# Performance work log

Hardware: AMD Instinct MI355X
Metric: run time of the kernel (lower is better)

## Reference

```python
import jax, jax.numpy as jnp
import numpy as np

N_SLOTS, KEY_DIM, VAL_DIM = 8192, 64, 64
B, S, TOPK = 8, 2048, 8


def setup_inputs() -> dict:
    key = jax.random.key(0)
    k1, k2, k3, k4, k5 = jax.random.split(key, 5)
    queries = jax.random.normal(k1, (B, S, KEY_DIM), dtype=jnp.float32)
    keys_mem = jax.random.normal(k2, (N_SLOTS, KEY_DIM), dtype=jnp.float32) * 0.02
    vals_mem = jax.random.normal(k3, (N_SLOTS, VAL_DIM), dtype=jnp.float32) * 0.02
    fast_vals = jax.random.normal(k4, (N_SLOTS, VAL_DIM), dtype=jnp.float32) * 0.01
    timestamps = jax.random.uniform(k5, (N_SLOTS,), dtype=jnp.float32)
    return {
        "queries": queries,
        "keys_mem": keys_mem,
        "vals_mem": vals_mem,
        "fast_vals": fast_vals,
        "timestamps": timestamps,
        "topk": TOPK,
    }


def reference(queries, keys_mem, vals_mem, fast_vals, timestamps, topk):
    # sim: [B, S, n_slots], scaled dot-product vs. memory keys
    scale = keys_mem.shape[1] ** (-0.5)
    sim = jnp.einsum("bsd,nd->bsn", queries, keys_mem) * scale
    # topk indices computed on detached scores (torch uses sim.detach())
    _, idx = jax.lax.top_k(jax.lax.stop_gradient(sim), topk)  # idx: [B, S, k]
    # gather topk similarities (torch does this via one-hot * sim; same math)
    sim_topk = jnp.take_along_axis(sim, idx, axis=-1)  # [B, S, k]
    # effective memory = slow + fast store; gather rows (torch: one_hot @ memory)
    effective_memory = vals_mem + fast_vals  # [n_slots, val_dim]
    gathered_vals = effective_memory[idx]  # [B, S, k, val_dim]
    attn_weights = jax.nn.softmax(sim_topk, axis=-1)  # [B, S, k]
    weighted_vals = gathered_vals * attn_weights[..., None]  # [B, S, k, val_dim]
    ts_retrieved = timestamps[idx]  # [B, S, k]
    return weighted_vals, idx, ts_retrieved
```

## Files before the change

### kernel.cpp

```cpp
#include <hip/hip_runtime.h>
#include <math.h>

#define NQ      16384
#define NSLOTS  8192
#define D       64
#define K       8

#define WV_ELEMS  (NQ * K * D)
#define IDX_OFF   (WV_ELEMS)
#define TSO_OFF   (IDX_OFF + NQ * K)

#define QPB_P   32
#define BLOCK_P 512
#define HALVES  2
#define SPW_P   (NSLOTS / HALVES / 8)
#define ITERS_P (SPW_P / 32)

#define QPB_R   16
#define BLOCK_R 256

#define POOL_SHORT_OFF 1572864
#define WS_NEED_NEW  (4u * 1024u * 1024u)
#define WS_NEED_OLD  (3u * 1024u * 1024u)

using short8   = __attribute__((ext_vector_type(8))) short;
using ushort8  = __attribute__((ext_vector_type(8))) unsigned short;
using bf16x8   = __attribute__((ext_vector_type(8))) __bf16;
using f32x4    = __attribute__((ext_vector_type(4))) float;

#define MFMA_BF16(A, B, C) __builtin_amdgcn_mfma_f32_16x16x32_bf16((A), (B), (C), 0, 0, 0)

__device__ __forceinline__ bf16x8 load_frag(const unsigned short* p) {
    short8 s = *reinterpret_cast<const short8*>(p);
    return __builtin_bit_cast(bf16x8, s);
}

__device__ __forceinline__ float packkey(float s, int code) {
    unsigned u = __float_as_uint(s) & 0xFFFFE000u;
    return __uint_as_float(u | (unsigned)code);
}

__device__ __forceinline__ void ins8(float (&tv)[8], float key) {
    float k2 = fmaxf(key, tv[0]);
    float o0 = fminf(tv[1], k2);
    float o1 = __builtin_amdgcn_fmed3f(tv[1], tv[2], k2);
    float o2 = __builtin_amdgcn_fmed3f(tv[2], tv[3], k2);
    float o3 = __builtin_amdgcn_fmed3f(tv[3], tv[4], k2);
    float o4 = __builtin_amdgcn_fmed3f(tv[4], tv[5], k2);
    float o5 = __builtin_amdgcn_fmed3f(tv[5], tv[6], k2);
    float o6 = __builtin_amdgcn_fmed3f(tv[6], tv[7], k2);
    float o7 = fmaxf(tv[7], k2);
    tv[0]=o0; tv[1]=o1; tv[2]=o2; tv[3]=o3; tv[4]=o4; tv[5]=o5; tv[6]=o6; tv[7]=o7;
}

__device__ __forceinline__ void cs(float& a, float& b) {
    const float lo = fminf(a, b), hi = fmaxf(a, b);
    a = lo; b = hi;
}
__device__ __forceinline__ void sort_bitonic8(float (&v)[8]) {
    cs(v[0],v[4]); cs(v[1],v[5]); cs(v[2],v[6]); cs(v[3],v[7]);
    cs(v[0],v[2]); cs(v[1],v[3]); cs(v[4],v[6]); cs(v[5],v[7]);
    cs(v[0],v[1]); cs(v[2],v[3]); cs(v[4],v[5]); cs(v[6],v[7]);
}

__device__ __forceinline__ void csu(unsigned long long& a, unsigned long long& b) {
    const bool lt = a < b;
    const unsigned long long lo = lt ? a : b;
    const unsigned long long hi = lt ? b : a;
    a = lo; b = hi;
}
__device__ __forceinline__ void sort_bitonic8_u64(unsigned long long (&v)[8]) {
    csu(v[0],v[4]); csu(v[1],v[5]); csu(v[2],v[6]); csu(v[3],v[7]);
    csu(v[0],v[2]); csu(v[1],v[3]); csu(v[4],v[6]); csu(v[5],v[7]);
    csu(v[0],v[1]); csu(v[2],v[3]); csu(v[4],v[5]); csu(v[6],v[7]);
}

__device__ __forceinline__ unsigned short f2bf(float f) {
    unsigned u = __float_as_uint(f);
    return (unsigned short)((u + 0x7FFFu + ((u >> 16) & 1u)) >> 16);
}

__global__ __launch_bounds__(256)
void conv_kernel(const float* __restrict__ q, const float* __restrict__ k,
                 unsigned short* __restrict__ ws) {
    const int t = blockIdx.x * blockDim.x + threadIdx.x;
    if (t < 262144) {
        float4 v = reinterpret_cast<const float4*>(q)[t];
        unsigned long long r =
              (unsigned long long)f2bf(v.x * 0.125f)
            | ((unsigned long long)f2bf(v.y * 0.125f) << 16)
            | ((unsigned long long)f2bf(v.z * 0.125f) << 32)
            | ((unsigned long long)f2bf(v.w * 0.125f) << 48);
        reinterpret_cast<unsigned long long*>(ws + 524288)[t] = r;
    } else if (t < 393216) {
        const int i = t - 262144;
        float4 v = reinterpret_cast<const float4*>(k)[i];
        unsigned long long r =
              (unsigned long long)f2bf(v.x)
            | ((unsigned long long)f2bf(v.y) << 16)
            | ((unsigned long long)f2bf(v.z) << 32)
            | ((unsigned long long)f2bf(v.w) << 48);
        reinterpret_cast<unsigned long long*>(ws)[i] = r;
    }
}

__global__ __launch_bounds__(BLOCK_P, 8)
void ltm_prefilter_kernel(const unsigned short* __restrict__ kb,
                          const unsigned short* __restrict__ qb,
                          unsigned short* __restrict__ poolu)
{
    __shared__ float candk[QPB_P][68];

    const int tid  = threadIdx.x;
    const int lane = tid & 63;
    const int w    = tid >> 6;
    const int row  = lane & 15;
    const int g    = lane >> 4;
    const int g4   = g * 4;
    const int koff = g * 8;
    const int bid  = blockIdx.x;
    const int qbase = (bid >> 1) * QPB_P;
    const int half  = bid & 1;

    const unsigned short* qpA = qb + (size_t)(qbase + row) * D + koff;
    const bf16x8 bA0 = load_frag(qpA);
    const bf16x8 bA1 = load_frag(qpA + 32);
    const bf16x8 bB0 = load_frag(qpA + 16 * D);
    const bf16x8 bB1 = load_frag(qpA + 16 * D + 32);

    float tvA[8], tvB[8];
    #pragma unroll
    for (int i = 0; i < 8; ++i) { tvA[i] = -INFINITY; tvB[i] = -INFINITY; }

    const int wbase = half * (NSLOTS / HALVES) + w * SPW_P;
    int codeA = 8191 - (wbase + g4);

    for (int it = 0; it < ITERS_P; ++it) {
        const int s0 = wbase + it * 32;
        const unsigned short* p = kb + (size_t)(s0 + row) * D + koff;
        const bf16x8 a00 = load_frag(p);
        const bf16x8 a01 = load_frag(p + 32);
        const bf16x8 a10 = load_frag(p + 16 * D);
        const bf16x8 a11 = load_frag(p + 16 * D + 32);

        const f32x4 z = {0.f, 0.f, 0.f, 0.f};
        f32x4 c00 = MFMA_BF16(a00, bA0, z);  c00 = MFMA_BF16(a01, bA1, c00);
        f32x4 c01 = MFMA_BF16(a00, bB0, z);  c01 = MFMA_BF16(a01, bB1, c01);
        f32x4 c10 = MFMA_BF16(a10, bA0, z);  c10 = MFMA_BF16(a11, bA1, c10);
        f32x4 c11 = MFMA_BF16(a10, bB0, z);  c11 = MFMA_BF16(a11, bB1, c11);

        ins8(tvA, packkey(c00[0], codeA     ));
        ins8(tvA, packkey(c00[1], codeA -  1));
        ins8(tvA, packkey(c00[2], codeA -  2));
        ins8(tvA, packkey(c00[3], codeA -  3));
        ins8(tvA, packkey(c10[0], codeA - 16));
        ins8(tvA, packkey(c10[1], codeA - 17));
        ins8(tvA, packkey(c10[2], codeA - 18));
        ins8(tvA, packkey(c10[3], codeA - 19));
        ins8(tvB, packkey(c01[0], codeA     ));
        ins8(tvB, packkey(c01[1], codeA -  1));
        ins8(tvB, packkey(c01[2], codeA -  2));
        ins8(tvB, packkey(c01[3], codeA -  3));
        ins8(tvB, packkey(c11[0], codeA - 16));
        ins8(tvB, packkey(c11[1], codeA - 17));
        ins8(tvB, packkey(c11[2], codeA - 18));
        ins8(tvB, packkey(c11[3], codeA - 19));

        codeA -= 32;
    }

    {
        float sA[8], sB[8];
        #pragma unroll
        for (int j = 0; j < 8; ++j) {
            sA[j] = __shfl_xor(tvA[j], 32, 64);
            sB[j] = __shfl_xor(tvB[j], 32, 64);
        }
        float mA[8], mB[8];
        #pragma unroll
        for (int j = 0; j < 8; ++j) {
            mA[j] = fmaxf(tvA[j], sA[7 - j]);
            mB[j] = fmaxf(tvB[j], sB[7 - j]);
        }
        sort_bitonic8(mA);
        sort_bitonic8(mB);
        #pragma unroll
        for (int j = 0; j < 8; ++j) {
            sA[j] = __shfl_xor(mA[j], 16, 64);
            sB[j] = __shfl_xor(mB[j], 16, 64);
        }
        float fA[8], fB[8];
        #pragma unroll
        for (int j = 0; j < 8; ++j) {
            fA[j] = fmaxf(mA[j], sA[7 - j]);
            fB[j] = fmaxf(mB[j], sB[7 - j]);
        }
        sort_bitonic8(fA);
        sort_bitonic8(fB);
        if (g == 0) {
            #pragma unroll
            for (int j = 0; j < 8; ++j) {
                candk[row     ][w * 8 + j] = fA[j];
                candk[row + 16][w * 8 + j] = fB[j];
            }
        }
    }
    __syncthreads();

    if (tid < 256) {
        const int  ql = tid >> 3;
        const int  jj = tid & 7;
        const bool hi = (jj & 1) != 0;

        float v[8];
        #pragma unroll
        for (int i = 0; i < 8; ++i) v[i] = candk[ql][jj * 8 + i];

        {
            float sk[8], mk[8];
            #pragma unroll
            for (int i = 0; i < 8; ++i) sk[i] = __shfl_xor(v[i], 1, 64);
            #pragma unroll
            for (int i = 0; i < 8; ++i)
                mk[i] = hi ? fmaxf(v[i], sk[7 - i]) : fminf(v[i], sk[7 - i]);
            sort_bitonic8(mk);
            #pragma unroll
            for (int i = 0; i < 8; ++i) v[i] = mk[i];
        }
        #pragma unroll
        for (int rnd = 0; rnd < 2; ++rnd) {
            const int st = rnd ? 5 : 3;
            float sk[8], mk[8], sk2[8];
            #pragma unroll
            for (int i = 0; i < 8; ++i) sk[i] = __shfl_xor(v[i], st, 64);
            #pragma unroll
            for (int i = 0; i < 8; ++i) mk[i] = fmaxf(v[i], sk[7 - i]);
            #pragma unroll
            for (int i = 0; i < 8; ++i) sk2[i] = __shfl_xor(mk[i], 1, 64);
            #pragma unroll
            for (int i = 0; i < 8; ++i)
                mk[i] = hi ? fmaxf(mk[i], sk2[i]) : fminf(mk[i], sk2[i]);
            sort_bitonic8(mk);
            #pragma unroll
            for (int i = 0; i < 8; ++i) v[i] = mk[i];
        }
        if (jj < 2) {
            ushort8 o;
            #pragma unroll
            for (int i = 0; i < 8; ++i)
                o[i] = (unsigned short)(8191u - (__float_as_uint(v[i]) & 8191u));
            *reinterpret_cast<ushort8*>(
                poolu + ((size_t)(qbase + ql) * 32 + half * 16 + jj * 8)) = o;
        }
    }
}

__global__ __launch_bounds__(BLOCK_R, 4)
void ltm_rescore_kernel(const float* __restrict__ queries,
                        const float* __restrict__ keys_mem,
                        const float* __restrict__ vals_mem,
                        const float* __restrict__ fast_vals,
                        const float* __restrict__ timestamps,
                        const unsigned short* __restrict__ poolu,
                        float* __restrict__ out)
{
    const int tid = threadIdx.x;
    const int ql  = tid >> 4;
    const int l16 = tid & 15;
    const int sg  = l16 >> 2;
    const int ls4 = l16 & 3;
    const int q   = blockIdx.x * QPB_R + ql;

    float4 qv4[4];
    {
        const float4* qp = reinterpret_cast<const float4*>(queries) + (size_t)q * 16 + ls4 * 4;
        #pragma unroll
        for (int i = 0; i < 4; ++i) qv4[i] = qp[i];
    }

    unsigned long long tk[8];
    #pragma unroll
    for (int i = 0; i < 8; ++i) tk[i] = 0ull;

    #pragma unroll 4
    for (int jt = 0; jt < 8; ++jt) {
        const int sid = poolu[(size_t)q * 32 + sg * 8 + jt];
        const float4* kp = reinterpret_cast<const float4*>(keys_mem) + (size_t)sid * 16 + ls4 * 4;
        float p = 0.f;
        #pragma unroll
        for (int i = 0; i < 4; ++i) {
            const float4 kc = kp[i];
            p = fmaf(qv4[i].x, kc.x, p);
            p = fmaf(qv4[i].y, kc.y, p);
            p = fmaf(qv4[i].z, kc.z, p);
            p = fmaf(qv4[i].w, kc.w, p);
        }
        p += __shfl_xor(p, 1, 64);
        p += __shfl_xor(p, 2, 64);
        const float s = p * 0.125f;
        const unsigned u  = __float_as_uint(s);
        const unsigned ou = (u & 0x80000000u) ? ~u : (u | 0x80000000u);
        const unsigned long long key =
            ((unsigned long long)ou << 13) | (unsigned)(8191 - sid);
        if (key > tk[0]) {
            tk[0] = key;
            #pragma unroll
            for (int uu = 0; uu < 7; ++uu) {
                const bool sw = tk[uu] > tk[uu + 1];
                const unsigned long long x = sw ? tk[uu + 1] : tk[uu];
                const unsigned long long y = sw ? tk[uu]     : tk[uu + 1];
                tk[uu] = x; tk[uu + 1] = y;
            }
        }
    }

    #pragma unroll
    for (int st = 4; st <= 8; st <<= 1) {
        unsigned long long sk[8], mk[8];
        #pragma unroll
        for (int j = 0; j < 8; ++j) sk[j] = __shfl_xor(tk[j], st, 64);
        #pragma unroll
        for (int j = 0; j < 8; ++j) {
            const unsigned long long a = tk[j], b = sk[7 - j];
            mk[j] = a > b ? a : b;
        }
        sort_bitonic8_u64(mk);
        #pragma unroll
        for (int j = 0; j < 8; ++j) tk[j] = mk[j];
    }

    float wv[K]; int wi[K];
    #pragma unroll
    for (int r = 0; r < K; ++r) {
        const unsigned long long best = tk[7 - r];
        const int      sid = 8191 - (int)(best & 8191ull);
        const unsigned ou  = (unsigned)(best >> 13);
        const unsigned ub  = (ou & 0x80000000u) ? (ou & 0x7FFFFFFFu) : ~ou;
        wv[r] = __uint_as_float(ub);
        wi[r] = sid;
    }
    const float m = wv[0];
    float e[K]; float sum = 0.f;
    #pragma unroll
    for (int r = 0; r < K; ++r) { e[r] = expf(wv[r] - m); sum += e[r]; }
    const float inv = 1.f / sum;

    {
        const int   r   = l16 >> 1;
        const int   h   = l16 & 1;
        const int   id  = wi[r];
        const float wgt = e[r] * inv;
        const float4* vp = reinterpret_cast<const float4*>(vals_mem)  + (size_t)id * 16 + h * 8;
        const float4* fp = reinterpret_cast<const float4*>(fast_vals) + (size_t)id * 16 + h * 8;
        float4* op = reinterpret_cast<float4*>(out) + ((size_t)(q * K + r)) * 16 + h * 8;
        #pragma unroll
        for (int i = 0; i < 8; ++i) {
            const float4 a = vp[i];
            const float4 b = fp[i];
            float4 c;
            c.x = (a.x + b.x) * wgt;
            c.y = (a.y + b.y) * wgt;
            c.z = (a.z + b.z) * wgt;
            c.w = (a.w + b.w) * wgt;
            op[i] = c;
        }
        if (l16 < 8) {
            out[IDX_OFF + (size_t)q * K + l16] = (float)wi[l16];
        } else {
            const int r2 = l16 - 8;
            out[TSO_OFF + (size_t)q * K + r2] = timestamps[wi[r2]];
        }
    }
}

#define QPB    32
#define BLOCK  512
#define WAVES  8
#define SPW    (NSLOTS / WAVES)
#define ITERS  (SPW / 32)

__global__ __launch_bounds__(BLOCK, 4)
void ltm_mfma_kernel(const float* __restrict__ queries,
                     const float* __restrict__ keys_mem,
                     const float* __restrict__ vals_mem,
                     const float* __restrict__ fast_vals,
                     const float* __restrict__ timestamps,
                     const unsigned short* __restrict__ kb,
                     const unsigned short* __restrict__ qb,
                     float* __restrict__ out)
{
    __shared__ float candk[QPB][68];

    const int tid  = threadIdx.x;
    const int lane = tid & 63;
    const int w    = tid >> 6;
    const int row  = lane & 15;
    const int g    = lane >> 4;
    const int g4   = g * 4;
    const int koff = g * 8;
    const int qbase = blockIdx.x * QPB;

    const unsigned short* qpA = qb + (size_t)(qbase + row) * D + koff;
    const bf16x8 bA0 = load_frag(qpA);
    const bf16x8 bA1 = load_frag(qpA + 32);
    const bf16x8 bB0 = load_frag(qpA + 16 * D);
    const bf16x8 bB1 = load_frag(qpA + 16 * D + 32);

    float tvA[8], tvB[8];
    #pragma unroll
    for (int i = 0; i < 8; ++i) { tvA[i] = -INFINITY; tvB[i] = -INFINITY; }

    const int wbase = w * SPW;
    const unsigned short* kp0 = kb + (size_t)(wbase + row) * D + koff;
    bf16x8 a00 = load_frag(kp0);
    bf16x8 a01 = load_frag(kp0 + 32);
    bf16x8 a10 = load_frag(kp0 + 16 * D);
    bf16x8 a11 = load_frag(kp0 + 16 * D + 32);

    int codeA = 8191 - (wbase + g4);

    #pragma unroll 2
    for (int it = 0; it < ITERS; ++it) {
        const int snext = wbase + (it + 1) * 32;
        const unsigned short* np_ = kb + (size_t)(snext + row) * D + koff;
        bf16x8 n00 = load_frag(np_);
        bf16x8 n01 = load_frag(np_ + 32);
        bf16x8 n10 = load_frag(np_ + 16 * D);
        bf16x8 n11 = load_frag(np_ + 16 * D + 32);

        const f32x4 z = {0.f, 0.f, 0.f, 0.f};
        f32x4 c00 = MFMA_BF16(a00, bA0, z);  c00 = MFMA_BF16(a01, bA1, c00);
        f32x4 c01 = MFMA_BF16(a00, bB0, z);  c01 = MFMA_BF16(a01, bB1, c01);
        f32x4 c10 = MFMA_BF16(a10, bA0, z);  c10 = MFMA_BF16(a11, bA1, c10);
        f32x4 c11 = MFMA_BF16(a10, bB0, z);  c11 = MFMA_BF16(a11, bB1, c11);

        ins8(tvA, packkey(c00[0], codeA     ));
        ins8(tvA, packkey(c00[1], codeA -  1));
        ins8(tvA, packkey(c00[2], codeA -  2));
        ins8(tvA, packkey(c00[3], codeA -  3));
        ins8(tvA, packkey(c10[0], codeA - 16));
        ins8(tvA, packkey(c10[1], codeA - 17));
        ins8(tvA, packkey(c10[2], codeA - 18));
        ins8(tvA, packkey(c10[3], codeA - 19));
        ins8(tvB, packkey(c01[0], codeA     ));
        ins8(tvB, packkey(c01[1], codeA -  1));
        ins8(tvB, packkey(c01[2], codeA -  2));
        ins8(tvB, packkey(c01[3], codeA -  3));
        ins8(tvB, packkey(c11[0], codeA - 16));
        ins8(tvB, packkey(c11[1], codeA - 17));
        ins8(tvB, packkey(c11[2], codeA - 18));
        ins8(tvB, packkey(c11[3], codeA - 19));

        codeA -= 32;
        a00 = n00; a01 = n01; a10 = n10; a11 = n11;
    }

    {
        float sA[8], sB[8];
        #pragma unroll
        for (int j = 0; j < 8; ++j) {
            sA[j] = __shfl_xor(tvA[j], 32, 64);
            sB[j] = __shfl_xor(tvB[j], 32, 64);
        }
        float mA[8], mB[8];
        #pragma unroll
        for (int j = 0; j < 8; ++j) {
            mA[j] = fmaxf(tvA[j], sA[7 - j]);
            mB[j] = fmaxf(tvB[j], sB[7 - j]);
        }
        sort_bitonic8(mA);
        sort_bitonic8(mB);
        #pragma unroll
        for (int j = 0; j < 8; ++j) {
            sA[j] = __shfl_xor(mA[j], 16, 64);
            sB[j] = __shfl_xor(mB[j], 16, 64);
        }
        if (g == 0) {
            #pragma unroll
            for (int j = 0; j < 8; ++j) {
                candk[row     ][w * 8 + j] = fmaxf(mA[j], sA[7 - j]);
                candk[row + 16][w * 8 + j] = fmaxf(mB[j], sB[7 - j]);
            }
        }
    }
    __syncthreads();

    const int ql  = tid >> 4;
    const int l16 = tid & 15;
    const int sg  = l16 >> 2;
    const int ls4 = l16 & 3;
    const int q   = qbase + ql;

    float4 qv4[4];
    {
        const float4* qp = reinterpret_cast<const float4*>(queries) + (size_t)q * 16 + ls4 * 4;
        #pragma unroll
        for (int i = 0; i < 4; ++i) qv4[i] = qp[i];
    }

    unsigned long long tk[8];
    #pragma unroll
    for (int i = 0; i < 8; ++i) tk[i] = 0ull;

    #pragma unroll 4
    for (int jt = 0; jt < 16; ++jt) {
        const float fk  = candk[ql][sg * 16 + jt];
        const int   sid = 8191 - (int)(__float_as_uint(fk) & 8191u);
        const float4* kp = reinterpret_cast<const float4*>(keys_mem) + (size_t)sid * 16 + ls4 * 4;
        float p = 0.f;
        #pragma unroll
        for (int i = 0; i < 4; ++i) {
            const float4 kc = kp[i];
            p = fmaf(qv4[i].x, kc.x, p);
            p = fmaf(qv4[i].y, kc.y, p);
            p = fmaf(qv4[i].z, kc.z, p);
            p = fmaf(qv4[i].w, kc.w, p);
        }
        p += __shfl_xor(p, 1, 64);
        p += __shfl_xor(p, 2, 64);
        const float s = p * 0.125f;
        const unsigned u  = __float_as_uint(s);
        const unsigned ou = (u & 0x80000000u) ? ~u : (u | 0x80000000u);
        const unsigned long long key =
            ((unsigned long long)ou << 13) | (unsigned)(8191 - sid);
        if (key > tk[0]) {
            tk[0] = key;
            #pragma unroll
            for (int uu = 0; uu < 7; ++uu) {
                const bool sw = tk[uu] > tk[uu + 1];
                const unsigned long long x = sw ? tk[uu + 1] : tk[uu];
                const unsigned long long y = sw ? tk[uu]     : tk[uu + 1];
                tk[uu] = x; tk[uu + 1] = y;
            }
        }
    }

    #pragma unroll
    for (int st = 4; st <= 8; st <<= 1) {
        unsigned long long sk[8], mk[8];
        #pragma unroll
        for (int j = 0; j < 8; ++j) sk[j] = __shfl_xor(tk[j], st, 64);
        #pragma unroll
        for (int j = 0; j < 8; ++j) {
            const unsigned long long a = tk[j], b = sk[7 - j];
            mk[j] = a > b ? a : b;
        }
        sort_bitonic8_u64(mk);
        #pragma unroll
        for (int j = 0; j < 8; ++j) tk[j] = mk[j];
    }

    float wv[K]; int wi[K];
    #pragma unroll
    for (int r = 0; r < K; ++r) {
        const unsigned long long best = tk[7 - r];
        const int      sid = 8191 - (int)(best & 8191ull);
        const unsigned ou  = (unsigned)(best >> 13);
        const unsigned ub  = (ou & 0x80000000u) ? (ou & 0x7FFFFFFFu) : ~ou;
        wv[r] = __uint_as_float(ub);
        wi[r] = sid;
    }
    const float m = wv[0];
    float e[K]; float sum = 0.f;
    #pragma unroll
    for (int r = 0; r < K; ++r) { e[r] = expf(wv[r] - m); sum += e[r]; }
    const float inv = 1.f / sum;

    {
        const int   r   = l16 >> 1;
        const int   h   = l16 & 1;
        const int   id  = wi[r];
        const float wgt = e[r] * inv;
        const float4* vp = reinterpret_cast<const float4*>(vals_mem)  + (size_t)id * 16 + h * 8;
        const float4* fp = reinterpret_cast<const float4*>(fast_vals) + (size_t)id * 16 + h * 8;
        float4* op = reinterpret_cast<float4*>(out) + ((size_t)(q * K + r)) * 16 + h * 8;
        #pragma unroll
        for (int i = 0; i < 8; ++i) {
            const float4 a = vp[i];
            const float4 b = fp[i];
            float4 c;
            c.x = (a.x + b.x) * wgt;
            c.y = (a.y + b.y) * wgt;
            c.z = (a.z + b.z) * wgt;
            c.w = (a.w + b.w) * wgt;
            op[i] = c;
        }
        if (l16 < 8) {
            out[IDX_OFF + (size_t)q * K + l16] = (float)wi[l16];
        } else {
            const int r2 = l16 - 8;
            out[TSO_OFF + (size_t)q * K + r2] = timestamps[wi[r2]];
        }
    }
}

#define FQPB   32
#define FTPQ   8
#define FBLOCK 256
#define FTS    128
#define FLDK   68
#define FNTILES (NSLOTS / FTS)

__global__ __launch_bounds__(FBLOCK, 2)
void ltm_fused_kernel(const float* __restrict__ queries,
                      const float* __restrict__ keys_mem,
                      const float* __restrict__ vals_mem,
                      const float* __restrict__ fast_vals,
                      const float* __restrict__ timestamps,
                      float* __restrict__ out)
{
    __shared__ float kt[FTS * FLDK];
    __shared__ float candv[FQPB][FTPQ * K];
    __shared__ int   candi[FQPB][FTPQ * K];
    __shared__ float selw[FQPB][K];
    __shared__ int   seli[FQPB][K];

    const int tid = threadIdx.x;
    const int ql  = tid / FTPQ;
    const int sub = tid % FTPQ;
    const int q   = blockIdx.x * FQPB + ql;

    float4 qv[D / 4];
    {
        const float4* qp = reinterpret_cast<const float4*>(queries + (size_t)q * D);
        #pragma unroll
        for (int i = 0; i < D / 4; ++i) qv[i] = qp[i];
    }

    float tv[K]; int ti[K];
    #pragma unroll
    for (int i = 0; i < K; ++i) { tv[i] = -INFINITY; ti[i] = 0; }

    for (int tile = 0; tile < FNTILES; ++tile) {
        __syncthreads();
        {
            const float4* kg = reinterpret_cast<const float4*>(keys_mem + (size_t)tile * FTS * D);
            #pragma unroll
            for (int i = 0; i < (FTS * D / 4) / FBLOCK; ++i) {
                const int e = tid + i * FBLOCK;
                const int row = e >> 4;
                const int col = e & 15;
                *reinterpret_cast<float4*>(&kt[row * FLDK + col * 4]) = kg[e];
            }
        }
        __syncthreads();

        #pragma unroll 4
        for (int j = 0; j < FTS / FTPQ; ++j) {
            const int local = sub + j * FTPQ;
            const float* kr = &kt[local * FLDK];
            float4 a0 = make_float4(0.f, 0.f, 0.f, 0.f);
            float4 a1 = make_float4(0.f, 0.f, 0.f, 0.f);
            #pragma unroll
            for (int i = 0; i < D / 4; i += 2) {
                const float4 k0 = *reinterpret_cast<const float4*>(&kr[(i + 0) * 4]);
                const float4 k1 = *reinterpret_cast<const float4*>(&kr[(i + 1) * 4]);
                a0.x = fmaf(k0.x, qv[i].x, a0.x);   a0.y = fmaf(k0.y, qv[i].y, a0.y);
                a0.z = fmaf(k0.z, qv[i].z, a0.z);   a0.w = fmaf(k0.w, qv[i].w, a0.w);
                a1.x = fmaf(k1.x, qv[i+1].x, a1.x); a1.y = fmaf(k1.y, qv[i+1].y, a1.y);
                a1.z = fmaf(k1.z, qv[i+1].z, a1.z); a1.w = fmaf(k1.w, qv[i+1].w, a1.w);
            }
            float s = ((a0.x + a1.x) + (a0.y + a1.y)) + ((a0.z + a1.z) + (a0.w + a1.w));
            s *= 0.125f;
            const int gid = tile * FTS + local;
            if (s > tv[0]) {
                tv[0] = s; ti[0] = gid;
                #pragma unroll
                for (int u = 0; u < K - 1; ++u) {
                    const bool sw = tv[u] > tv[u + 1];
                    const float va = sw ? tv[u + 1] : tv[u];
                    const float vb = sw ? tv[u]     : tv[u + 1];
                    const int   ia = sw ? ti[u + 1] : ti[u];
                    const int   ib = sw ? ti[u]     : ti[u + 1];
                    tv[u] = va; tv[u + 1] = vb; ti[u] = ia; ti[u + 1] = ib;
                }
            }
        }
    }

    #pragma unroll
    for (int i = 0; i < K; ++i) {
        candv[ql][sub * K + i] = tv[i];
        candi[ql][sub * K + i] = ti[i];
    }
    __syncthreads();

    if (sub == 0) {
        float wv[K]; int wi[K];
        #pragma unroll
        for (int r = 0; r < K; ++r) {
            float bv = -INFINITY; int bi = 0x7fffffff; int bp = 0;
            for (int c = 0; c < FTPQ * K; ++c) {
                const float v = candv[ql][c];
                const int  id = candi[ql][c];
                if ((v > bv) || (v == bv && id < bi)) { bv = v; bi = id; bp = c; }
            }
            candv[ql][bp] = -INFINITY;
            wv[r] = bv; wi[r] = bi;
        }
        const float m = wv[0];
        float e[K]; float sum = 0.f;
        #pragma unroll
        for (int r = 0; r < K; ++r) { e[r] = expf(wv[r] - m); sum += e[r]; }
        const float inv = 1.f / sum;
        #pragma unroll
        for (int r = 0; r < K; ++r) { selw[ql][r] = e[r] * inv; seli[ql][r] = wi[r]; }
    }
    __syncthreads();

    {
        const int r = sub;
        const int id = seli[ql][r];
        const float w = selw[ql][r];
        const float4* vp = reinterpret_cast<const float4*>(vals_mem  + (size_t)id * D);
        const float4* fp = reinterpret_cast<const float4*>(fast_vals + (size_t)id * D);
        float4* op = reinterpret_cast<float4*>(out + (size_t)(q * K + r) * D);
        #pragma unroll
        for (int i = 0; i < D / 4; ++i) {
            const float4 a = vp[i];
            const float4 b = fp[i];
            float4 c;
            c.x = (a.x + b.x) * w; c.y = (a.y + b.y) * w;
            c.z = (a.z + b.z) * w; c.w = (a.w + b.w) * w;
            op[i] = c;
        }
        out[IDX_OFF + (size_t)q * K + r] = (float)id;
        out[TSO_OFF + (size_t)q * K + r] = timestamps[id];
    }
}

extern "C" void kernel_launch(void* const* d_in, const int* in_sizes, int n_in,
                              void* d_out, int out_size, void* d_ws, size_t ws_size,
                              hipStream_t stream) {
    (void)in_sizes; (void)n_in; (void)out_size;
    const float* queries    = (const float*)d_in[0];
    const float* keys_mem   = (const float*)d_in[1];
    const float* vals_mem   = (const float*)d_in[2];
    const float* fast_vals  = (const float*)d_in[3];
    const float* timestamps = (const float*)d_in[4];
    float* out = (float*)d_out;

    if (ws_size >= WS_NEED_NEW) {
        unsigned short* ws = (unsigned short*)d_ws;
        unsigned short* poolu = ws + POOL_SHORT_OFF;
        conv_kernel<<<1536, 256, 0, stream>>>(queries, keys_mem, ws);
        ltm_prefilter_kernel<<<(NQ / QPB_P) * HALVES, BLOCK_P, 0, stream>>>(
            ws , ws + 524288 , poolu);
        ltm_rescore_kernel<<<NQ / QPB_R, BLOCK_R, 0, stream>>>(
            queries, keys_mem, vals_mem, fast_vals, timestamps, poolu, out);
    } else if (ws_size >= WS_NEED_OLD) {
        unsigned short* ws = (unsigned short*)d_ws;
        conv_kernel<<<1536, 256, 0, stream>>>(queries, keys_mem, ws);
        ltm_mfma_kernel<<<NQ / QPB, BLOCK, 0, stream>>>(
            queries, keys_mem, vals_mem, fast_vals, timestamps,
            ws , ws + 524288 , out);
    } else {
        ltm_fused_kernel<<<NQ / FQPB, FBLOCK, 0, stream>>>(
            queries, keys_mem, vals_mem, fast_vals, timestamps, out);
    }
}
```

Measured before the change: 112.2 us.

## Prefetch next key fragments in MFMA scan and sort rescored candidates with network

The MFMA similarity scan now loads the next iteration's bf16 key fragments before computing on the current ones, and the loop is unrolled by 2. This is meant to hide global-load latency behind the MFMA and top-k insert work. In the rescoring kernel, the per-candidate conditional insertion is replaced by building all 8 keys and then sorting them once with a fixed 19-comparator network, which removes the branches. The prefetch reads one block of rows past the end of each wave's range on the last iteration, which costs extra registers and an out-of-range read.

```diff
diff --git a/kernel.cpp b/kernel.cpp
--- a/kernel.cpp
+++ b/kernel.cpp
@@ -73,6 +73,14 @@
     csu(v[0],v[4]); csu(v[1],v[5]); csu(v[2],v[6]); csu(v[3],v[7]);
     csu(v[0],v[2]); csu(v[1],v[3]); csu(v[4],v[6]); csu(v[5],v[7]);
     csu(v[0],v[1]); csu(v[2],v[3]); csu(v[4],v[5]); csu(v[6],v[7]);
+}
+__device__ __forceinline__ void sort8_u64(unsigned long long (&v)[8]) {
+    csu(v[0],v[1]); csu(v[2],v[3]); csu(v[4],v[5]); csu(v[6],v[7]);
+    csu(v[0],v[2]); csu(v[1],v[3]); csu(v[4],v[6]); csu(v[5],v[7]);
+    csu(v[1],v[2]); csu(v[5],v[6]);
+    csu(v[0],v[4]); csu(v[1],v[5]); csu(v[2],v[6]); csu(v[3],v[7]);
+    csu(v[2],v[4]); csu(v[3],v[5]);
+    csu(v[1],v[2]); csu(v[3],v[4]); csu(v[5],v[6]);
 }
 
 __device__ __forceinline__ unsigned short f2bf(float f) {
@@ -133,15 +141,23 @@
     for (int i = 0; i < 8; ++i) { tvA[i] = -INFINITY; tvB[i] = -INFINITY; }
 
     const int wbase = half * (NSLOTS / HALVES) + w * SPW_P;
+
+    const unsigned short* kp0 = kb + (size_t)(wbase + row) * D + koff;
+    bf16x8 a00 = load_frag(kp0);
+    bf16x8 a01 = load_frag(kp0 + 32);
+    bf16x8 a10 = load_frag(kp0 + 16 * D);
+    bf16x8 a11 = load_frag(kp0 + 16 * D + 32);
+
     int codeA = 8191 - (wbase + g4);
 
+    #pragma unroll 2
     for (int it = 0; it < ITERS_P; ++it) {
-        const int s0 = wbase + it * 32;
-        const unsigned short* p = kb + (size_t)(s0 + row) * D + koff;
-        const bf16x8 a00 = load_frag(p);
-        const bf16x8 a01 = load_frag(p + 32);
-        const bf16x8 a10 = load_frag(p + 16 * D);
-        const bf16x8 a11 = load_frag(p + 16 * D + 32);
+        const int snext = wbase + (it + 1) * 32;
+        const unsigned short* np_ = kb + (size_t)(snext + row) * D + koff;
+        bf16x8 n00 = load_frag(np_);
+        bf16x8 n01 = load_frag(np_ + 32);
+        bf16x8 n10 = load_frag(np_ + 16 * D);
+        bf16x8 n11 = load_frag(np_ + 16 * D + 32);
 
         const f32x4 z = {0.f, 0.f, 0.f, 0.f};
         f32x4 c00 = MFMA_BF16(a00, bA0, z);  c00 = MFMA_BF16(a01, bA1, c00);
@@ -167,6 +183,7 @@
         ins8(tvB, packkey(c11[3], codeA - 19));
 
         codeA -= 32;
+        a00 = n00; a01 = n01; a10 = n10; a11 = n11;
     }
 
     {
@@ -280,9 +297,6 @@
 
     unsigned long long tk[8];
     #pragma unroll
-    for (int i = 0; i < 8; ++i) tk[i] = 0ull;
-
-    #pragma unroll 4
     for (int jt = 0; jt < 8; ++jt) {
         const int sid = poolu[(size_t)q * 32 + sg * 8 + jt];
         const float4* kp = reinterpret_cast<const float4*>(keys_mem) + (size_t)sid * 16 + ls4 * 4;
@@ -300,19 +314,9 @@
         const float s = p * 0.125f;
         const unsigned u  = __float_as_uint(s);
         const unsigned ou = (u & 0x80000000u) ? ~u : (u | 0x80000000u);
-        const unsigned long long key =
-            ((unsigned long long)ou << 13) | (unsigned)(8191 - sid);
-        if (key > tk[0]) {
-            tk[0] = key;
-            #pragma unroll
-            for (int uu = 0; uu < 7; ++uu) {
-                const bool sw = tk[uu] > tk[uu + 1];
-                const unsigned long long x = sw ? tk[uu + 1] : tk[uu];
-                const unsigned long long y = sw ? tk[uu]     : tk[uu + 1];
-                tk[uu] = x; tk[uu + 1] = y;
-            }
-        }
-    }
+        tk[jt] = ((unsigned long long)ou << 13) | (unsigned)(8191 - sid);
+    }
+    sort8_u64(tk);
 
     #pragma unroll
     for (int st = 4; st <= 8; st <<= 1) {
```

Result: no change. 112.2 us (+0.1%).

## Split prefilter top-8 trackers and widen rescore to 32 lanes per query

Applied to the files above, without the earlier changes.

The prefilter kernel now keeps four independent top-8 lists per lane instead of two, merging them with a bitonic step after the loop. This shortens the serial insert dependency chains and exposes more instruction-level parallelism, at the cost of more registers, so its occupancy hint drops from 8 to 6. The rescore kernel now gives each query 32 lanes instead of 16: each lane scores 4 candidates, sorts them with a small network rather than conditional insertion, and takes one extra shuffle-merge stage. The value gather and weighting are spread across 4 lanes per output row, and that kernel's occupancy hint rises to 8.

```diff
diff --git a/kernel.cpp b/kernel.cpp
--- a/kernel.cpp
+++ b/kernel.cpp
@@ -16,7 +16,7 @@
 #define SPW_P   (NSLOTS / HALVES / 8)
 #define ITERS_P (SPW_P / 32)
 
-#define QPB_R   16
+#define QPB_R   8
 #define BLOCK_R 256
 
 #define POOL_SHORT_OFF 1572864
@@ -104,7 +104,7 @@
     }
 }
 
-__global__ __launch_bounds__(BLOCK_P, 8)
+__global__ __launch_bounds__(BLOCK_P, 6)
 void ltm_prefilter_kernel(const unsigned short* __restrict__ kb,
                           const unsigned short* __restrict__ qb,
                           unsigned short* __restrict__ poolu)
@@ -128,9 +128,12 @@
     const bf16x8 bB0 = load_frag(qpA + 16 * D);
     const bf16x8 bB1 = load_frag(qpA + 16 * D + 32);
 
-    float tvA[8], tvB[8];
-    #pragma unroll
-    for (int i = 0; i < 8; ++i) { tvA[i] = -INFINITY; tvB[i] = -INFINITY; }
+    float tvA0[8], tvA1[8], tvB0[8], tvB1[8];
+    #pragma unroll
+    for (int i = 0; i < 8; ++i) {
+        tvA0[i] = -INFINITY; tvA1[i] = -INFINITY;
+        tvB0[i] = -INFINITY; tvB1[i] = -INFINITY;
+    }
 
     const int wbase = half * (NSLOTS / HALVES) + w * SPW_P;
     int codeA = 8191 - (wbase + g4);
@@ -149,25 +152,34 @@
         f32x4 c10 = MFMA_BF16(a10, bA0, z);  c10 = MFMA_BF16(a11, bA1, c10);
         f32x4 c11 = MFMA_BF16(a10, bB0, z);  c11 = MFMA_BF16(a11, bB1, c11);
 
-        ins8(tvA, packkey(c00[0], codeA     ));
-        ins8(tvA, packkey(c00[1], codeA -  1));
-        ins8(tvA, packkey(c00[2], codeA -  2));
-        ins8(tvA, packkey(c00[3], codeA -  3));
-        ins8(tvA, packkey(c10[0], codeA - 16));
-        ins8(tvA, packkey(c10[1], codeA - 17));
-        ins8(tvA, packkey(c10[2], codeA - 18));
-        ins8(tvA, packkey(c10[3], codeA - 19));
-        ins8(tvB, packkey(c01[0], codeA     ));
-        ins8(tvB, packkey(c01[1], codeA -  1));
-        ins8(tvB, packkey(c01[2], codeA -  2));
-        ins8(tvB, packkey(c01[3], codeA -  3));
-        ins8(tvB, packkey(c11[0], codeA - 16));
-        ins8(tvB, packkey(c11[1], codeA - 17));
-        ins8(tvB, packkey(c11[2], codeA - 18));
-        ins8(tvB, packkey(c11[3], codeA - 19));
+        ins8(tvA0, packkey(c00[0], codeA     ));
+        ins8(tvA0, packkey(c00[1], codeA -  1));
+        ins8(tvA0, packkey(c00[2], codeA -  2));
+        ins8(tvA0, packkey(c00[3], codeA -  3));
+        ins8(tvA1, packkey(c10[0], codeA - 16));
+        ins8(tvA1, packkey(c10[1], codeA - 17));
+        ins8(tvA1, packkey(c10[2], codeA - 18));
+        ins8(tvA1, packkey(c10[3], codeA - 19));
+        ins8(tvB0, packkey(c01[0], codeA     ));
+        ins8(tvB0, packkey(c01[1], codeA -  1));
+        ins8(tvB0, packkey(c01[2], codeA -  2));
+        ins8(tvB0, packkey(c01[3], codeA -  3));
+        ins8(tvB1, packkey(c11[0], codeA - 16));
+        ins8(tvB1, packkey(c11[1], codeA - 17));
+        ins8(tvB1, packkey(c11[2], codeA - 18));
+        ins8(tvB1, packkey(c11[3], codeA - 19));
 
         codeA -= 32;
     }
+
+    float tvA[8], tvB[8];
+    #pragma unroll
+    for (int j = 0; j < 8; ++j) {
+        tvA[j] = fmaxf(tvA0[j], tvA1[7 - j]);
+        tvB[j] = fmaxf(tvB0[j], tvB1[7 - j]);
+    }
+    sort_bitonic8(tvA);
+    sort_bitonic8(tvB);
 
     {
         float sA[8], sB[8];
@@ -255,7 +267,7 @@
     }
 }
 
-__global__ __launch_bounds__(BLOCK_R, 4)
+__global__ __launch_bounds__(BLOCK_R, 8)
 void ltm_rescore_kernel(const float* __restrict__ queries,
                         const float* __restrict__ keys_mem,
                         const float* __restrict__ vals_mem,
@@ -265,10 +277,10 @@
                         float* __restrict__ out)
 {
     const int tid = threadIdx.x;
-    const int ql  = tid >> 4;
-    const int l16 = tid & 15;
-    const int sg  = l16 >> 2;
-    const int ls4 = l16 & 3;
+    const int ql  = tid >> 5;
+    const int l32 = tid & 31;
+    const int sg  = l32 >> 2;
+    const int ls4 = l32 & 3;
     const int q   = blockIdx.x * QPB_R + ql;
 
     float4 qv4[4];
@@ -278,13 +290,10 @@
         for (int i = 0; i < 4; ++i) qv4[i] = qp[i];
     }
 
-    unsigned long long tk[8];
-    #pragma unroll
-    for (int i = 0; i < 8; ++i) tk[i] = 0ull;
-
-    #pragma unroll 4
-    for (int jt = 0; jt < 8; ++jt) {
-        const int sid = poolu[(size_t)q * 32 + sg * 8 + jt];
+    unsigned long long kk[4];
+    #pragma unroll
+    for (int jt = 0; jt < 4; ++jt) {
+        const int sid = poolu[(size_t)q * 32 + sg * 4 + jt];
         const float4* kp = reinterpret_cast<const float4*>(keys_mem) + (size_t)sid * 16 + ls4 * 4;
         float p = 0.f;
         #pragma unroll
@@ -300,22 +309,17 @@
         const float s = p * 0.125f;
         const unsigned u  = __float_as_uint(s);
         const unsigned ou = (u & 0x80000000u) ? ~u : (u | 0x80000000u);
-        const unsigned long long key =
-            ((unsigned long long)ou << 13) | (unsigned)(8191 - sid);
-        if (key > tk[0]) {
-            tk[0] = key;
-            #pragma unroll
-            for (int uu = 0; uu < 7; ++uu) {
-                const bool sw = tk[uu] > tk[uu + 1];
-                const unsigned long long x = sw ? tk[uu + 1] : tk[uu];
-                const unsigned long long y = sw ? tk[uu]     : tk[uu + 1];
-                tk[uu] = x; tk[uu + 1] = y;
-            }
-        }
-    }
-
-    #pragma unroll
-    for (int st = 4; st <= 8; st <<= 1) {
+        kk[jt] = ((unsigned long long)ou << 13) | (unsigned)(8191 - sid);
+    }
+    csu(kk[0], kk[1]); csu(kk[2], kk[3]);
+    csu(kk[0], kk[2]); csu(kk[1], kk[3]);
+    csu(kk[1], kk[2]);
+    unsigned long long tk[8];
+    tk[0] = 0ull; tk[1] = 0ull; tk[2] = 0ull; tk[3] = 0ull;
+    tk[4] = kk[0]; tk[5] = kk[1]; tk[6] = kk[2]; tk[7] = kk[3];
+
+    #pragma unroll
+    for (int st = 4; st <= 16; st <<= 1) {
         unsigned long long sk[8], mk[8];
         #pragma unroll
         for (int j = 0; j < 8; ++j) sk[j] = __shfl_xor(tk[j], st, 64);
@@ -346,15 +350,15 @@
     const float inv = 1.f / sum;
 
     {
-        const int   r   = l16 >> 1;
-        const int   h   = l16 & 1;
+        const int   r   = l32 >> 2;
+        const int   s4  = l32 & 3;
         const int   id  = wi[r];
         const float wgt = e[r] * inv;
-        const float4* vp = reinterpret_cast<const float4*>(vals_mem)  + (size_t)id * 16 + h * 8;
-        const float4* fp = reinterpret_cast<const float4*>(fast_vals) + (size_t)id * 16 + h * 8;
-        float4* op = reinterpret_cast<float4*>(out) + ((size_t)(q * K + r)) * 16 + h * 8;
-        #pragma unroll
-        for (int i = 0; i < 8; ++i) {
+        const float4* vp = reinterpret_cast<const float4*>(vals_mem)  + (size_t)id * 16 + s4 * 4;
+        const float4* fp = reinterpret_cast<const float4*>(fast_vals) + (size_t)id * 16 + s4 * 4;
+        float4* op = reinterpret_cast<float4*>(out) + ((size_t)(q * K + r)) * 16 + s4 * 4;
+        #pragma unroll
+        for (int i = 0; i < 4; ++i) {
             const float4 a = vp[i];
             const float4 b = fp[i];
             float4 c;
@@ -364,10 +368,10 @@
             c.w = (a.w + b.w) * wgt;
             op[i] = c;
         }
-        if (l16 < 8) {
-            out[IDX_OFF + (size_t)q * K + l16] = (float)wi[l16];
-        } else {
-            const int r2 = l16 - 8;
+        if (l32 < 8) {
+            out[IDX_OFF + (size_t)q * K + l32] = (float)wi[l32];
+        } else if (l32 < 16) {
+            const int r2 = l32 - 8;
             out[TSO_OFF + (size_t)q * K + r2] = timestamps[wi[r2]];
         }
     }
```

After: 112.3 us. No clear change (+0.2%).
